# Performance work log

Hardware: AMD Instinct MI355X
Metric: run time of the kernel (lower is better)

Reference implementation:

```python
import jax, jax.numpy as jnp
import numpy as np

B, N, D_IN, D_OUT, H = 2, 2048, 1024, 1024, 16
HD = D_OUT // H


def setup_inputs() -> dict:
    key = jax.random.key(0)
    ks = jax.random.split(key, 6)
    s_in = 1.0 / np.sqrt(D_IN)
    s_out = 1.0 / np.sqrt(D_OUT)
    return {
        "x": jax.random.normal(ks[0], (B, N, D_IN), dtype=jnp.float32),
        "Wq": jax.random.uniform(ks[1], (D_IN, D_OUT), jnp.float32, -s_in, s_in),
        "Wk": jax.random.uniform(ks[2], (D_IN, D_OUT), jnp.float32, -s_in, s_in),
        "Wv": jax.random.uniform(ks[3], (D_IN, D_OUT), jnp.float32, -s_in, s_in),
        "Wo": jax.random.uniform(ks[4], (D_OUT, D_OUT), jnp.float32, -s_out, s_out),
        "bo": jax.random.uniform(ks[5], (D_OUT,), jnp.float32, -s_out, s_out),
    }


def reference(x, Wq, Wk, Wv, Wo, bo):
    b, n, _ = x.shape
    # project and split heads: [b, n, d_out] -> [b, h, n, hd]
    def heads(w):
        return w.reshape(b, n, H, HD).transpose(0, 2, 1, 3)
    q = heads(x @ Wq)
    k = heads(x @ Wk)
    v = heads(x @ Wv)
    # materialized causal attention (dropout rate 0.0 -> identity)
    scores = jnp.einsum("bhqd,bhkd->bhqk", q, k)
    causal = jnp.tril(jnp.ones((n, n), dtype=bool))  # keep lower triangle
    scores = jnp.where(causal, scores, -jnp.inf)
    attn = jax.nn.softmax(scores / np.sqrt(HD), axis=-1)
    ctx = jnp.einsum("bhqk,bhkd->bhqd", attn, v)
    ctx = ctx.transpose(0, 2, 1, 3).reshape(b, n, D_OUT)
    return ctx @ Wo + bo
```

## Files before the change

kernel.cpp:

```cpp
#include <hip/hip_runtime.h>
#include <math.h>
#include <stdint.h>

#define B_ 2
#define N_ 2048
#define D_ 1024
#define H_ 16
#define HD_ 64
#define M_ (B_ * N_)

typedef __bf16 bf16x8 __attribute__((ext_vector_type(8)));
typedef float f32x4 __attribute__((ext_vector_type(4)));

__device__ __forceinline__ ushort bfbits(float f) {
    __bf16 h = (__bf16)f;
    return __builtin_bit_cast(ushort, h);
}

__device__ __forceinline__ void glds16(const ushort* g, ushort* l) {
    __builtin_amdgcn_global_load_lds(
        (const __attribute__((address_space(1))) uint32_t*)g,
        (__attribute__((address_space(3))) uint32_t*)l, 16, 0, 0);
}

__global__ __launch_bounds__(256) void prep(const float* __restrict__ x,
                                            const float* __restrict__ W0,
                                            const float* __restrict__ W1,
                                            const float* __restrict__ W2,
                                            const float* __restrict__ W3,
                                            ushort* __restrict__ xb,
                                            ushort* __restrict__ Wt) {
    __shared__ float T[32][33];
    const int t = threadIdx.x;
    int id = blockIdx.x;
    if (id < 4096) {
        int i = id * 256 + t;
        float4 v = ((const float4*)x)[i];
        ushort4 o;
        o.x = bfbits(v.x); o.y = bfbits(v.y); o.z = bfbits(v.z); o.w = bfbits(v.w);
        ((ushort4*)xb)[i] = o;
        return;
    }
    id -= 4096;
    const int z = id >> 10;
    const int k0 = (id & 31) * 32, n0 = ((id >> 5) & 31) * 32;
    const float* W = (z == 0) ? W0 : (z == 1) ? W1 : (z == 2) ? W2 : W3;
    ushort* out = Wt + (size_t)z * D_ * D_;
    {
        int kl = t >> 3, nl = (t & 7) * 4;
        float4 v = *(const float4*)&W[(size_t)(k0 + kl) * D_ + n0 + nl];
        T[kl][nl] = v.x; T[kl][nl + 1] = v.y; T[kl][nl + 2] = v.z; T[kl][nl + 3] = v.w;
    }
    __syncthreads();
    {
        int nl = t >> 3, k4 = (t & 7) * 4;
        ushort4 o;
        o.x = bfbits(T[k4 + 0][nl]); o.y = bfbits(T[k4 + 1][nl]);
        o.z = bfbits(T[k4 + 2][nl]); o.w = bfbits(T[k4 + 3][nl]);
        *(ushort4*)&out[(size_t)(n0 + nl) * D_ + k0 + k4] = o;
    }
}

#define BK 32

__device__ __forceinline__ void gemm_tile(const ushort* __restrict__ A,
                                          const ushort* __restrict__ Bt,
                                          int K, int tileM, int tileN,
                                          ushort* As, ushort* Bs,
                                          f32x4 acc[4][4]) {
    const int t = threadIdx.x;
    const int l = t & 63;
    const int w = __builtin_amdgcn_readfirstlane(t >> 6);
    const int wr = w >> 1, wc = w & 1;
    const int li = l & 15, lg = l >> 4;
    const int lr = l >> 2;
    const int colu = (((l & 3) ^ (lr & 3)) << 3);
    const int swz = (li & 3) << 3;

    for (int k0 = 0; k0 < K; k0 += BK) {
        __syncthreads();
        #pragma unroll
        for (int it = 0; it < 2; ++it) {
            const int c2 = it * 4 + w;
            const int row = c2 * 16 + lr;
            glds16(&A[(size_t)(tileM + row) * K + k0 + colu], &As[c2 * 512]);
            glds16(&Bt[(size_t)(tileN + row) * K + k0 + colu], &Bs[c2 * 512]);
        }
        __syncthreads();
        bf16x8 a[4], b[4];
        #pragma unroll
        for (int m = 0; m < 4; ++m)
            a[m] = *(const bf16x8*)&As[(wr * 64 + m * 16 + li) * 32 + ((lg << 3) ^ swz)];
        #pragma unroll
        for (int n = 0; n < 4; ++n)
            b[n] = *(const bf16x8*)&Bs[(wc * 64 + n * 16 + li) * 32 + ((lg << 3) ^ swz)];
        #pragma unroll
        for (int m = 0; m < 4; ++m)
            #pragma unroll
            for (int n = 0; n < 4; ++n)
                acc[m][n] = __builtin_amdgcn_mfma_f32_16x16x32_bf16(a[m], b[n], acc[m][n], 0, 0, 0);
    }
}

#define QSCALE 0.180336880f

__global__ __launch_bounds__(256) void qkv_gemm(const ushort* __restrict__ xb,
                                                const ushort* __restrict__ Wt,
                                                ushort* __restrict__ q,
                                                ushort* __restrict__ k,
                                                ushort* __restrict__ vt) {
    __shared__ ushort As[128 * 32];
    __shared__ ushort Bs[128 * 32];
    __shared__ ushort Eps[128][130];
    f32x4 acc[4][4];
    #pragma unroll
    for (int m = 0; m < 4; ++m)
        #pragma unroll
        for (int n = 0; n < 4; ++n)
            acc[m][n] = (f32x4){0.f, 0.f, 0.f, 0.f};

    const int wg = (blockIdx.x & 7) * 96 + (blockIdx.x >> 3);
    const int tileM = (wg & 31) * 128;
    const int yy = wg >> 5;
    const int wsel = yy >> 3;
    const int tileN = (yy & 7) * 128;
    const ushort* Bmat = Wt + (size_t)wsel * D_ * D_;

    gemm_tile(xb, Bmat, D_, tileM, tileN, As, Bs, acc);

    const int t = threadIdx.x;
    const int l = t & 63, w = t >> 6;
    const int wr = w >> 1, wc = w & 1;
    const int li = l & 15, lg = l >> 4;
    const float scale = (wsel == 0) ? QSCALE : 1.0f;

    if (wsel < 2) {
        #pragma unroll
        for (int m = 0; m < 4; ++m)
            #pragma unroll
            for (int n = 0; n < 4; ++n)
                #pragma unroll
                for (int r = 0; r < 4; ++r)
                    Eps[wr * 64 + m * 16 + lg * 4 + r][wc * 64 + n * 16 + li] =
                        bfbits(acc[m][n][r] * scale);
    } else {
        #pragma unroll
        for (int m = 0; m < 4; ++m)
            #pragma unroll
            for (int n = 0; n < 4; ++n)
                #pragma unroll
                for (int r = 0; r < 4; ++r)
                    Eps[wc * 64 + n * 16 + li][wr * 64 + m * 16 + lg * 4 + r] =
                        bfbits(acc[m][n][r]);
    }
    __syncthreads();

    const int rr = t >> 3;
    const int cb = (t & 7) * 16;
    if (wsel < 2) {
        ushort* out = (wsel == 0) ? q : k;
        #pragma unroll
        for (int it = 0; it < 4; ++it) {
            const int row = it * 32 + rr;
            uint4 v0 = *(const uint4*)&Eps[row][cb];
            uint4 v1 = *(const uint4*)&Eps[row][cb + 8];
            size_t base = (size_t)(tileM + row) * D_ + tileN + cb;
            *(uint4*)&out[base] = v0;
            *(uint4*)&out[base + 8] = v1;
        }
    } else {
        const int b = tileM >> 11;
        const int n0 = (tileM & (N_ - 1)) + cb;
        #pragma unroll
        for (int it = 0; it < 4; ++it) {
            const int row = it * 32 + rr;
            const int gcol = tileN + row;
            const int h = gcol >> 6, hd = gcol & 63;
            uint4 v0 = *(const uint4*)&Eps[row][cb];
            uint4 v1 = *(const uint4*)&Eps[row][cb + 8];
            size_t base = ((size_t)(b * H_ + h) * HD_ + hd) * N_ + n0;
            *(uint4*)&vt[base] = v0;
            *(uint4*)&vt[base + 8] = v1;
        }
    }
}

__global__ __launch_bounds__(256) void out_gemm(const ushort* __restrict__ ctx,
                                                const ushort* __restrict__ Wt,
                                                const float* __restrict__ bo,
                                                float* __restrict__ outp) {
    __shared__ ushort As[128 * 32];
    __shared__ ushort Bs[128 * 32];
    f32x4 acc[4][4];
    #pragma unroll
    for (int m = 0; m < 4; ++m)
        #pragma unroll
        for (int n = 0; n < 4; ++n)
            acc[m][n] = (f32x4){0.f, 0.f, 0.f, 0.f};

    const int wg = (blockIdx.x & 7) * 32 + (blockIdx.x >> 3);
    const int tileM = (wg & 31) * 128;
    const int tileN = (wg >> 5) * 128;
    const ushort* Bmat = Wt + (size_t)3 * D_ * D_;

    gemm_tile(ctx, Bmat, D_, tileM, tileN, As, Bs, acc);

    const int l = threadIdx.x & 63, w = threadIdx.x >> 6;
    const int wr = w >> 1, wc = w & 1;
    const int li = l & 15, lg = l >> 4;
    #pragma unroll
    for (int n = 0; n < 4; ++n) {
        float bias = bo[tileN + wc * 64 + n * 16 + li];
        #pragma unroll
        for (int m = 0; m < 4; ++m)
            #pragma unroll
            for (int r = 0; r < 4; ++r) {
                int grow = tileM + wr * 64 + m * 16 + lg * 4 + r;
                int gcol = tileN + wc * 64 + n * 16 + li;
                outp[(size_t)grow * D_ + gcol] = acc[m][n][r] + bias;
            }
    }
}

__device__ __forceinline__ void qk_mfma(f32x4 st[4], const ushort* Kb,
                                        const bf16x8 bq[2],
                                        int li, int lg, int rswz) {
    #pragma unroll
    for (int c = 0; c < 4; ++c) {
        st[c] = (f32x4){0.f, 0.f, 0.f, 0.f};
        #pragma unroll
        for (int tk = 0; tk < 2; ++tk) {
            bf16x8 kf = *(const bf16x8*)&Kb[(c * 16 + li) * 64 + (((tk * 4 + lg) ^ rswz) * 8)];
            st[c] = __builtin_amdgcn_mfma_f32_16x16x32_bf16(kf, bq[tk], st[c], 0, 0, 0);
        }
    }
}

__device__ __forceinline__ void softmax_pv(f32x4 st[4], const ushort* Vb,
                                           bool masked, int jkb, int qg,
                                           int li, int lg, int rswz,
                                           ushort* PsW, f32x4& lacc,
                                           f32x4 od[4], bf16x8 ones) {
    if (masked) {
        #pragma unroll
        for (int c = 0; c < 4; ++c)
            #pragma unroll
            for (int r = 0; r < 4; ++r) {
                const int kgl = jkb * 64 + c * 16 + lg * 4 + r;
                if (kgl > qg) st[c][r] = -INFINITY;
            }
    }
    const int sw = li & 7;
    #pragma unroll
    for (int c = 0; c < 4; ++c) {
        float p0 = exp2f(st[c][0]);
        float p1 = exp2f(st[c][1]);
        float p2 = exp2f(st[c][2]);
        float p3 = exp2f(st[c][3]);
        uint32_t w0, w1;
        asm("v_cvt_pk_bf16_f32 %0, %1, %2" : "=v"(w0) : "v"(p0), "v"(p1));
        asm("v_cvt_pk_bf16_f32 %0, %1, %2" : "=v"(w1) : "v"(p2), "v"(p3));
        uint2 pk; pk.x = w0; pk.y = w1;
        *(uint2*)&PsW[li * 64 + (((c * 2 + (lg >> 1)) ^ sw) << 3) + ((lg & 1) << 2)] = pk;
    }
    #pragma unroll
    for (int tj = 0; tj < 2; ++tj) {
        bf16x8 pa = *(const bf16x8*)&PsW[li * 64 + (((tj * 4 + lg) ^ sw) << 3)];
        lacc = __builtin_amdgcn_mfma_f32_16x16x32_bf16(pa, ones, lacc, 0, 0, 0);
        #pragma unroll
        for (int db = 0; db < 4; ++db) {
            bf16x8 bv = *(const bf16x8*)&Vb[(db * 16 + li) * 64 + (((tj * 4 + lg) ^ rswz) * 8)];
            od[db] = __builtin_amdgcn_mfma_f32_16x16x32_bf16(pa, bv, od[db], 0, 0, 0);
        }
    }
}

__global__ __launch_bounds__(256, 2) void attn_fwd(const ushort* __restrict__ q,
                                                   const ushort* __restrict__ k,
                                                   const ushort* __restrict__ vt,
                                                   ushort* __restrict__ ctx) {
    __shared__ ushort Ks[2][4096];
    __shared__ ushort Vs[2][4096];
    __shared__ ushort Ps[4][1024];

    const int t = threadIdx.x;
    const int l = t & 63;
    const int w = __builtin_amdgcn_readfirstlane(t >> 6);
    const int li = l & 15, lg = l >> 4;
    const int f = blockIdx.x;
    const int bh = ((f & 7) << 2) | ((f >> 3) & 3);
    const int p = f >> 5;
    const int qtA = p, qtB = 31 - p;
    const int b = bh >> 4, h = bh & 15;

    const ushort* Qg = q + ((size_t)b * N_) * D_ + h * 64;
    const ushort* Kg = k + ((size_t)b * N_) * D_ + h * 64;
    const ushort* Vg = vt + (size_t)bh * HD_ * N_;
    ushort* PsW = &Ps[w][0];

    const int r8 = l >> 3;
    const int soff = ((l & 7) ^ r8) * 8;
    const int rswz = li & 7;

    const int qgA = qtA * 64 + w * 16 + li;
    const int qgB = qtB * 64 + w * 16 + li;

    bf16x8 bqA[2], bqB[2];
    #pragma unroll
    for (int tk = 0; tk < 2; ++tk) {
        bqA[tk] = *(const bf16x8*)&Qg[(size_t)qgA * D_ + tk * 32 + lg * 8];
        bqB[tk] = *(const bf16x8*)&Qg[(size_t)qgB * D_ + tk * 32 + lg * 8];
    }

    bf16x8 ones;
    #pragma unroll
    for (int i = 0; i < 8; ++i) ones[i] = (__bf16)1.0f;

    f32x4 odA[4], odB[4];
    #pragma unroll
    for (int db = 0; db < 4; ++db) {
        odA[db] = (f32x4){0.f, 0.f, 0.f, 0.f};
        odB[db] = (f32x4){0.f, 0.f, 0.f, 0.f};
    }
    f32x4 laccA = (f32x4){0.f, 0.f, 0.f, 0.f};
    f32x4 laccB = (f32x4){0.f, 0.f, 0.f, 0.f};

    #pragma unroll
    for (int i = 0; i < 2; ++i) {
        const int seg = w + i * 4;
        const int row = seg * 8 + r8;
        glds16(&Kg[(size_t)row * D_ + soff], &Ks[0][seg * 512]);
        glds16(&Vg[(size_t)row * N_ + soff], &Vs[0][seg * 512]);
    }
    __syncthreads();

    int cur = 0;
    for (int kb = 0; kb <= qtB; ++kb) {
        if (kb < qtB) {
            #pragma unroll
            for (int i = 0; i < 2; ++i) {
                const int seg = w + i * 4;
                const int row = seg * 8 + r8;
                glds16(&Kg[(size_t)((kb + 1) * 64 + row) * D_ + soff], &Ks[cur ^ 1][seg * 512]);
                glds16(&Vg[(size_t)row * N_ + (kb + 1) * 64 + soff], &Vs[cur ^ 1][seg * 512]);
            }
        }
        {
            f32x4 st[4];
            qk_mfma(st, Ks[cur], bqB, li, lg, rswz);
            softmax_pv(st, Vs[cur], kb == qtB, kb, qgB, li, lg, rswz, PsW, laccB, odB, ones);
        }
        if (kb <= qtA) {
            f32x4 st[4];
            qk_mfma(st, Ks[cur], bqA, li, lg, rswz);
            softmax_pv(st, Vs[cur], kb == qtA, kb, qgA, li, lg, rswz, PsW, laccA, odA, ones);
        }
        __syncthreads();
        cur ^= 1;
    }

    #pragma unroll
    for (int r = 0; r < 4; ++r) {
        const float invA = 1.f / laccA[r];
        const int growA = qtA * 64 + w * 16 + lg * 4 + r;
        #pragma unroll
        for (int db = 0; db < 4; ++db)
            ctx[((size_t)(b * N_ + growA)) * D_ + h * 64 + db * 16 + li] = bfbits(odA[db][r] * invA);
        const float invB = 1.f / laccB[r];
        const int growB = qtB * 64 + w * 16 + lg * 4 + r;
        #pragma unroll
        for (int db = 0; db < 4; ++db)
            ctx[((size_t)(b * N_ + growB)) * D_ + h * 64 + db * 16 + li] = bfbits(odB[db][r] * invB);
    }
}

extern "C" void kernel_launch(void* const* d_in, const int* in_sizes, int n_in,
                              void* d_out, int out_size, void* d_ws, size_t ws_size,
                              hipStream_t stream) {
    (void)in_sizes; (void)n_in; (void)out_size; (void)ws_size;
    const float* x  = (const float*)d_in[0];
    const float* Wq = (const float*)d_in[1];
    const float* Wk = (const float*)d_in[2];
    const float* Wv = (const float*)d_in[3];
    const float* Wo = (const float*)d_in[4];
    const float* bo = (const float*)d_in[5];
    float* outp = (float*)d_out;

    ushort* xb  = (ushort*)d_ws;
    ushort* Wt  = xb + (size_t)M_ * D_;
    ushort* qb  = Wt + (size_t)4 * D_ * D_;
    ushort* kb  = qb + (size_t)M_ * D_;
    ushort* vtb = kb + (size_t)M_ * D_;
    ushort* ctx = vtb + (size_t)M_ * D_;

    prep<<<dim3(8192), 256, 0, stream>>>(x, Wq, Wk, Wv, Wo, xb, Wt);
    qkv_gemm<<<dim3(768), 256, 0, stream>>>(xb, Wt, qb, kb, vtb);
    attn_fwd<<<dim3(512), 256, 0, stream>>>(qb, kb, vtb, ctx);
    out_gemm<<<dim3(256), 256, 0, stream>>>(ctx, Wt, bo, outp);
}
```

Baseline: 106.8 us.

## Replace QKV GEMM with 256x256 double-buffered 8-wave pipelined kernel

Replaces the 128x128 single-buffered QKV projection with a 256x256-tile, 512-thread kernel. It double-buffers K=64 LDS stages and interleaves global-to-LDS loads with MFMA phases using sched barriers and s_setprio. V is computed directly as Wv^T·x^T so the transposed layout comes out of the GEMM without an LDS transpose epilogue. The larger tiles give more reuse per byte and hide load latency. The trade-off is only 192 workgroups on a GPU with 256 CUs, and uncoalesced scalar 2-byte stores in the epilogue.

```diff
diff --git a/kernel.cpp b/kernel.cpp
--- a/kernel.cpp
+++ b/kernel.cpp
@@ -61,6 +61,166 @@
     }
 }
 
+#define QSCALE 0.180336880f
+
+#define STG(SRC, RB, K0, DST, HALF)                                            \
+    do {                                                                       \
+        glds16(&SRC[(size_t)((RB) + (HALF) * 128 + w * 8 + r8) * 1024 + (K0) + s8], \
+               &DST[((HALF) * 128 + w * 8) * 64]);                             \
+        glds16(&SRC[(size_t)((RB) + (HALF) * 128 + (w + 8) * 8 + r8) * 1024 + (K0) + s8], \
+               &DST[((HALF) * 128 + (w + 8) * 8) * 64]);                       \
+    } while (0)
+
+#define DS_READS(KT, MH, TK)                                                   \
+    _Pragma("unroll") for (int mi = 0; mi < 4; ++mi)                           \
+        af[mi] = *(const bf16x8*)&LA[KT][(wr * 128 + ((MH) * 4 + mi) * 16 + li) * 64 + \
+                                         ((((TK) * 4 + lg) ^ rsw) << 3)];      \
+    _Pragma("unroll") for (int nj = 0; nj < 4; ++nj)                           \
+        bfr[nj] = *(const bf16x8*)&LB[KT][(wc * 64 + nj * 16 + li) * 64 +      \
+                                          ((((TK) * 4 + lg) ^ rsw) << 3)];
+
+#define MFMA16(MH)                                                             \
+    __builtin_amdgcn_s_setprio(1);                                             \
+    _Pragma("unroll") for (int mi = 0; mi < 4; ++mi)                           \
+        _Pragma("unroll") for (int nj = 0; nj < 4; ++nj)                       \
+            acc[(MH) * 4 + mi][nj] = __builtin_amdgcn_mfma_f32_16x16x32_bf16(  \
+                af[mi], bfr[nj], acc[(MH) * 4 + mi][nj], 0, 0, 0);             \
+    __builtin_amdgcn_s_setprio(0);
+
+#define BARF()                                                                 \
+    __builtin_amdgcn_sched_barrier(0);                                         \
+    __builtin_amdgcn_s_barrier();                                              \
+    __builtin_amdgcn_sched_barrier(0)
+
+__global__ __launch_bounds__(512, 2) void qkv8_gemm(const ushort* __restrict__ xb,
+                                                    const ushort* __restrict__ Wt,
+                                                    ushort* __restrict__ q,
+                                                    ushort* __restrict__ k,
+                                                    ushort* __restrict__ vt) {
+    __shared__ ushort LA[2][256 * 64];
+    __shared__ ushort LB[2][256 * 64];
+
+    const int t = threadIdx.x;
+    const int l = t & 63;
+    const int w = __builtin_amdgcn_readfirstlane(t >> 6);
+    const int wr = w >> 2, wc = w & 3;
+    const int li = l & 15, lg = l >> 4;
+    const int r8 = l >> 3;
+    const int s8 = ((l & 7) ^ r8) * 8;
+    const int rsw = li & 7;
+
+    const int wg = (blockIdx.x & 7) * 24 + (blockIdx.x >> 3);
+    const int op = wg >> 6;
+    const int rr_ = wg & 63;
+    const ushort* Asrc; const ushort* Bsrc;
+    int rowbase, colbase;
+    if (op < 2) {
+        Asrc = xb; Bsrc = Wt + (size_t)op * D_ * D_;
+        rowbase = (rr_ & 15) * 256;
+        colbase = (rr_ >> 4) * 256;
+    } else {
+        Asrc = Wt + (size_t)2 * D_ * D_;
+        Bsrc = xb;
+        rowbase = (rr_ & 3) * 256;
+        colbase = (rr_ >> 2) * 256;
+    }
+
+    f32x4 acc[8][4];
+    #pragma unroll
+    for (int m = 0; m < 8; ++m)
+        #pragma unroll
+        for (int n = 0; n < 4; ++n)
+            acc[m][n] = (f32x4){0.f, 0.f, 0.f, 0.f};
+
+    STG(Asrc, rowbase, 0, LA[0], 0);  STG(Asrc, rowbase, 0, LA[0], 1);
+    STG(Bsrc, colbase, 0, LB[0], 0);  STG(Bsrc, colbase, 0, LB[0], 1);
+    STG(Asrc, rowbase, 64, LA[1], 0); STG(Asrc, rowbase, 64, LA[1], 1);
+    STG(Bsrc, colbase, 64, LB[1], 0); STG(Bsrc, colbase, 64, LB[1], 1);
+
+    #pragma unroll 1
+    for (int it = 0; it < 8; ++it) {
+        const int kT1 = it * 128 + 64;
+        const int kN0 = it * 128 + 128;
+        const int kN1 = it * 128 + 192;
+        bf16x8 af[4], bfr[4];
+
+        if (it > 0) STG(Asrc, rowbase, kT1, LA[1], 1);
+        asm volatile("s_waitcnt vmcnt(4)" ::: "memory");
+        BARF();
+        DS_READS(0, 0, 0);
+        MFMA16(0);
+        BARF();
+        DS_READS(0, 0, 1);
+        if (it > 0) STG(Bsrc, colbase, kT1, LB[1], 0);
+        BARF();
+        MFMA16(0);
+        BARF();
+        DS_READS(0, 1, 0);
+        if (it > 0) STG(Bsrc, colbase, kT1, LB[1], 1);
+        BARF();
+        MFMA16(1);
+        BARF();
+        DS_READS(0, 1, 1);
+        if (it < 7) STG(Asrc, rowbase, kN0, LA[0], 0);
+        BARF();
+        MFMA16(1);
+        BARF();
+        if (it < 7) {
+            STG(Asrc, rowbase, kN0, LA[0], 1);
+            asm volatile("s_waitcnt vmcnt(4)" ::: "memory");
+        } else {
+            asm volatile("s_waitcnt vmcnt(0)" ::: "memory");
+        }
+        BARF();
+        DS_READS(1, 0, 0);
+        MFMA16(0);
+        BARF();
+        DS_READS(1, 0, 1);
+        if (it < 7) STG(Bsrc, colbase, kN0, LB[0], 0);
+        BARF();
+        MFMA16(0);
+        BARF();
+        DS_READS(1, 1, 0);
+        if (it < 7) STG(Bsrc, colbase, kN0, LB[0], 1);
+        BARF();
+        MFMA16(1);
+        BARF();
+        DS_READS(1, 1, 1);
+        if (it < 7) STG(Asrc, rowbase, kN1, LA[1], 0);
+        BARF();
+        MFMA16(1);
+        BARF();
+    }
+
+    if (op < 2) {
+        ushort* out = (op == 0) ? q : k;
+        const float scale = (op == 0) ? QSCALE : 1.0f;
+        #pragma unroll
+        for (int m = 0; m < 8; ++m)
+            #pragma unroll
+            for (int n = 0; n < 4; ++n)
+                #pragma unroll
+                for (int r = 0; r < 4; ++r) {
+                    const int grow = rowbase + wr * 128 + m * 16 + lg * 4 + r;
+                    const int gcol = colbase + wc * 64 + n * 16 + li;
+                    out[(size_t)grow * D_ + gcol] = bfbits(acc[m][n][r] * scale);
+                }
+    } else {
+        const int bb = colbase >> 11;
+        const int tcb = colbase & (N_ - 1);
+        #pragma unroll
+        for (int m = 0; m < 8; ++m)
+            #pragma unroll
+            for (int n = 0; n < 4; ++n)
+                #pragma unroll
+                for (int r = 0; r < 4; ++r) {
+                    const int drow = rowbase + wr * 128 + m * 16 + lg * 4 + r;
+                    const int tcol = tcb + wc * 64 + n * 16 + li;
+                    vt[((size_t)(bb * 1024 + drow)) * N_ + tcol] = bfbits(acc[m][n][r]);
+                }
+    }
+}
+
 #define BK 32
 
 __device__ __forceinline__ void gemm_tile(const ushort* __restrict__ A,
@@ -102,89 +262,6 @@
     }
 }
 
-#define QSCALE 0.180336880f
-
-__global__ __launch_bounds__(256) void qkv_gemm(const ushort* __restrict__ xb,
-                                                const ushort* __restrict__ Wt,
-                                                ushort* __restrict__ q,
-                                                ushort* __restrict__ k,
-                                                ushort* __restrict__ vt) {
-    __shared__ ushort As[128 * 32];
-    __shared__ ushort Bs[128 * 32];
-    __shared__ ushort Eps[128][130];
-    f32x4 acc[4][4];
-    #pragma unroll
-    for (int m = 0; m < 4; ++m)
-        #pragma unroll
-        for (int n = 0; n < 4; ++n)
-            acc[m][n] = (f32x4){0.f, 0.f, 0.f, 0.f};
-
-    const int wg = (blockIdx.x & 7) * 96 + (blockIdx.x >> 3);
-    const int tileM = (wg & 31) * 128;
-    const int yy = wg >> 5;
-    const int wsel = yy >> 3;
-    const int tileN = (yy & 7) * 128;
-    const ushort* Bmat = Wt + (size_t)wsel * D_ * D_;
-
-    gemm_tile(xb, Bmat, D_, tileM, tileN, As, Bs, acc);
-
-    const int t = threadIdx.x;
-    const int l = t & 63, w = t >> 6;
-    const int wr = w >> 1, wc = w & 1;
-    const int li = l & 15, lg = l >> 4;
-    const float scale = (wsel == 0) ? QSCALE : 1.0f;
-
-    if (wsel < 2) {
-        #pragma unroll
-        for (int m = 0; m < 4; ++m)
-            #pragma unroll
-            for (int n = 0; n < 4; ++n)
-                #pragma unroll
-                for (int r = 0; r < 4; ++r)
-                    Eps[wr * 64 + m * 16 + lg * 4 + r][wc * 64 + n * 16 + li] =
-                        bfbits(acc[m][n][r] * scale);
-    } else {
-        #pragma unroll
-        for (int m = 0; m < 4; ++m)
-            #pragma unroll
-            for (int n = 0; n < 4; ++n)
-                #pragma unroll
-                for (int r = 0; r < 4; ++r)
-                    Eps[wc * 64 + n * 16 + li][wr * 64 + m * 16 + lg * 4 + r] =
-                        bfbits(acc[m][n][r]);
-    }
-    __syncthreads();
-
-    const int rr = t >> 3;
-    const int cb = (t & 7) * 16;
-    if (wsel < 2) {
-        ushort* out = (wsel == 0) ? q : k;
-        #pragma unroll
-        for (int it = 0; it < 4; ++it) {
-            const int row = it * 32 + rr;
-            uint4 v0 = *(const uint4*)&Eps[row][cb];
-            uint4 v1 = *(const uint4*)&Eps[row][cb + 8];
-            size_t base = (size_t)(tileM + row) * D_ + tileN + cb;
-            *(uint4*)&out[base] = v0;
-            *(uint4*)&out[base + 8] = v1;
-        }
-    } else {
-        const int b = tileM >> 11;
-        const int n0 = (tileM & (N_ - 1)) + cb;
-        #pragma unroll
-        for (int it = 0; it < 4; ++it) {
-            const int row = it * 32 + rr;
-            const int gcol = tileN + row;
-            const int h = gcol >> 6, hd = gcol & 63;
-            uint4 v0 = *(const uint4*)&Eps[row][cb];
-            uint4 v1 = *(const uint4*)&Eps[row][cb + 8];
-            size_t base = ((size_t)(b * H_ + h) * HD_ + hd) * N_ + n0;
-            *(uint4*)&vt[base] = v0;
-            *(uint4*)&vt[base + 8] = v1;
-        }
-    }
-}
-
 __global__ __launch_bounds__(256) void out_gemm(const ushort* __restrict__ ctx,
                                                 const ushort* __restrict__ Wt,
                                                 const float* __restrict__ bo,
@@ -394,7 +471,7 @@
     ushort* ctx = vtb + (size_t)M_ * D_;
 
     prep<<<dim3(8192), 256, 0, stream>>>(x, Wq, Wk, Wv, Wo, xb, Wt);
-    qkv_gemm<<<dim3(768), 256, 0, stream>>>(xb, Wt, qb, kb, vtb);
+    qkv8_gemm<<<dim3(192), 512, 0, stream>>>(xb, Wt, qb, kb, vtb);
     attn_fwd<<<dim3(512), 256, 0, stream>>>(qb, kb, vtb, ctx);
     out_gemm<<<dim3(256), 256, 0, stream>>>(ctx, Wt, bo, outp);
 }
```

Measured after the change: 109.3 us. 1.02x slower.

## Triple-buffer K/V tiles in attention with partial vmcnt waits

Applied to the files above, without the earlier changes.

Moves the attention kernel's K/V LDS staging from a double buffer to a triple buffer, prefetching two tiles ahead. It replaces the full __syncthreads with explicit s_waitcnt vmcnt(4)/vmcnt(0) plus a raw barrier, so loads for the next tile can stay in flight across the barrier. The P scratch buffer is split per query tile (A/B) so the two softmax passes don't share LDS. This raises LDS use per block, which may reduce occupancy relative to the launch bound of 2 blocks per CU.

```diff
diff --git a/kernel.cpp b/kernel.cpp
--- a/kernel.cpp
+++ b/kernel.cpp
@@ -222,6 +222,12 @@
     }
 }
 
+#define WAITV4() do { asm volatile("s_waitcnt vmcnt(4)" ::: "memory"); } while (0)
+#define WAITV0() do { asm volatile("s_waitcnt vmcnt(0)" ::: "memory"); } while (0)
+#define SBAR()  do { __builtin_amdgcn_sched_barrier(0); \
+                     __builtin_amdgcn_s_barrier(); \
+                     __builtin_amdgcn_sched_barrier(0); } while (0)
+
 __device__ __forceinline__ void qk_mfma(f32x4 st[4], const ushort* Kb,
                                         const bf16x8 bq[2],
                                         int li, int lg, int rswz) {
@@ -279,9 +285,9 @@
                                                    const ushort* __restrict__ k,
                                                    const ushort* __restrict__ vt,
                                                    ushort* __restrict__ ctx) {
-    __shared__ ushort Ks[2][4096];
-    __shared__ ushort Vs[2][4096];
-    __shared__ ushort Ps[4][1024];
+    __shared__ ushort Ks[3][4096];
+    __shared__ ushort Vs[3][4096];
+    __shared__ ushort Ps[2][4][1024];
 
     const int t = threadIdx.x;
     const int l = t & 63;
@@ -296,7 +302,8 @@
     const ushort* Qg = q + ((size_t)b * N_) * D_ + h * 64;
     const ushort* Kg = k + ((size_t)b * N_) * D_ + h * 64;
     const ushort* Vg = vt + (size_t)bh * HD_ * N_;
-    ushort* PsW = &Ps[w][0];
+    ushort* PsB = &Ps[0][w][0];
+    ushort* PsA = &Ps[1][w][0];
 
     const int r8 = l >> 3;
     const int soff = ((l & 7) ^ r8) * 8;
@@ -326,37 +333,43 @@
     f32x4 laccB = (f32x4){0.f, 0.f, 0.f, 0.f};
 
     #pragma unroll
-    for (int i = 0; i < 2; ++i) {
-        const int seg = w + i * 4;
-        const int row = seg * 8 + r8;
-        glds16(&Kg[(size_t)row * D_ + soff], &Ks[0][seg * 512]);
-        glds16(&Vg[(size_t)row * N_ + soff], &Vs[0][seg * 512]);
-    }
-    __syncthreads();
-
-    int cur = 0;
+    for (int s = 0; s < 2; ++s)
+        #pragma unroll
+        for (int i = 0; i < 2; ++i) {
+            const int seg = w + i * 4;
+            const int row = seg * 8 + r8;
+            glds16(&Kg[(size_t)(s * 64 + row) * D_ + soff], &Ks[s][seg * 512]);
+            glds16(&Vg[(size_t)row * N_ + s * 64 + soff], &Vs[s][seg * 512]);
+        }
+    WAITV4();
+    SBAR();
+
     for (int kb = 0; kb <= qtB; ++kb) {
-        if (kb < qtB) {
+        const int rd = kb % 3;
+        if (kb + 2 <= qtB) {
+            const int st = (kb + 2) % 3;
             #pragma unroll
             for (int i = 0; i < 2; ++i) {
                 const int seg = w + i * 4;
                 const int row = seg * 8 + r8;
-                glds16(&Kg[(size_t)((kb + 1) * 64 + row) * D_ + soff], &Ks[cur ^ 1][seg * 512]);
-                glds16(&Vg[(size_t)row * N_ + (kb + 1) * 64 + soff], &Vs[cur ^ 1][seg * 512]);
+                glds16(&Kg[(size_t)((kb + 2) * 64 + row) * D_ + soff], &Ks[st][seg * 512]);
+                glds16(&Vg[(size_t)row * N_ + (kb + 2) * 64 + soff], &Vs[st][seg * 512]);
             }
         }
         {
-            f32x4 st[4];
-            qk_mfma(st, Ks[cur], bqB, li, lg, rswz);
-            softmax_pv(st, Vs[cur], kb == qtB, kb, qgB, li, lg, rswz, PsW, laccB, odB, ones);
+            f32x4 st4[4];
+            qk_mfma(st4, Ks[rd], bqB, li, lg, rswz);
+            softmax_pv(st4, Vs[rd], kb == qtB, kb, qgB, li, lg, rswz, PsB, laccB, odB, ones);
         }
         if (kb <= qtA) {
-            f32x4 st[4];
-            qk_mfma(st, Ks[cur], bqA, li, lg, rswz);
-            softmax_pv(st, Vs[cur], kb == qtA, kb, qgA, li, lg, rswz, PsW, laccA, odA, ones);
-        }
-        __syncthreads();
-        cur ^= 1;
+            f32x4 st4[4];
+            qk_mfma(st4, Ks[rd], bqA, li, lg, rswz);
+            softmax_pv(st4, Vs[rd], kb == qtA, kb, qgA, li, lg, rswz, PsA, laccA, odA, ones);
+        }
+        if (kb < qtB) {
+            if (kb + 2 <= qtB) WAITV4(); else WAITV0();
+            SBAR();
+        }
     }
 
     #pragma unroll
```

New measurement: 107.5 us. Within noise of the previous version (+0.7%).

## Split paired causal query tiles across 8 waves instead of serial per-wave processing

Applied to the files above, without the earlier changes.

The attention kernel previously had each of 4 waves process two query tiles (p and 31-p) serially for load balance. Now blocks use 512 threads: waves 0-3 handle the long tile and waves 4-7 the short tile, sharing the same double-buffered K/V LDS tiles, with each wave loading one K/V segment. This halves per-wave register state and doubles parallelism per block, but the short-tile waves sit idle at barriers once their tile finishes.

```diff
diff --git a/kernel.cpp b/kernel.cpp
--- a/kernel.cpp
+++ b/kernel.cpp
@@ -275,13 +275,13 @@
     }
 }
 
-__global__ __launch_bounds__(256, 2) void attn_fwd(const ushort* __restrict__ q,
+__global__ __launch_bounds__(512, 4) void attn_fwd(const ushort* __restrict__ q,
                                                    const ushort* __restrict__ k,
                                                    const ushort* __restrict__ vt,
                                                    ushort* __restrict__ ctx) {
     __shared__ ushort Ks[2][4096];
     __shared__ ushort Vs[2][4096];
-    __shared__ ushort Ps[4][1024];
+    __shared__ ushort Ps[8][1024];
 
     const int t = threadIdx.x;
     const int l = t & 63;
@@ -290,8 +290,9 @@
     const int f = blockIdx.x;
     const int bh = ((f & 7) << 2) | ((f >> 3) & 3);
     const int p = f >> 5;
-    const int qtA = p, qtB = 31 - p;
     const int b = bh >> 4, h = bh & 15;
+    const int wl = w & 3;
+    const int myqt = (w < 4) ? (31 - p) : p;
 
     const ushort* Qg = q + ((size_t)b * N_) * D_ + h * 64;
     const ushort* Kg = k + ((size_t)b * N_) * D_ + h * 64;
@@ -299,61 +300,41 @@
     ushort* PsW = &Ps[w][0];
 
     const int r8 = l >> 3;
+    const int srow = w * 8 + r8;
     const int soff = ((l & 7) ^ r8) * 8;
     const int rswz = li & 7;
 
-    const int qgA = qtA * 64 + w * 16 + li;
-    const int qgB = qtB * 64 + w * 16 + li;
-
-    bf16x8 bqA[2], bqB[2];
-    #pragma unroll
-    for (int tk = 0; tk < 2; ++tk) {
-        bqA[tk] = *(const bf16x8*)&Qg[(size_t)qgA * D_ + tk * 32 + lg * 8];
-        bqB[tk] = *(const bf16x8*)&Qg[(size_t)qgB * D_ + tk * 32 + lg * 8];
-    }
+    const int qg = myqt * 64 + wl * 16 + li;
+
+    bf16x8 bq[2];
+    #pragma unroll
+    for (int tk = 0; tk < 2; ++tk)
+        bq[tk] = *(const bf16x8*)&Qg[(size_t)qg * D_ + tk * 32 + lg * 8];
 
     bf16x8 ones;
     #pragma unroll
     for (int i = 0; i < 8; ++i) ones[i] = (__bf16)1.0f;
 
-    f32x4 odA[4], odB[4];
-    #pragma unroll
-    for (int db = 0; db < 4; ++db) {
-        odA[db] = (f32x4){0.f, 0.f, 0.f, 0.f};
-        odB[db] = (f32x4){0.f, 0.f, 0.f, 0.f};
-    }
-    f32x4 laccA = (f32x4){0.f, 0.f, 0.f, 0.f};
-    f32x4 laccB = (f32x4){0.f, 0.f, 0.f, 0.f};
-
-    #pragma unroll
-    for (int i = 0; i < 2; ++i) {
-        const int seg = w + i * 4;
-        const int row = seg * 8 + r8;
-        glds16(&Kg[(size_t)row * D_ + soff], &Ks[0][seg * 512]);
-        glds16(&Vg[(size_t)row * N_ + soff], &Vs[0][seg * 512]);
-    }
+    f32x4 od[4];
+    #pragma unroll
+    for (int db = 0; db < 4; ++db) od[db] = (f32x4){0.f, 0.f, 0.f, 0.f};
+    f32x4 lacc = (f32x4){0.f, 0.f, 0.f, 0.f};
+
+    glds16(&Kg[(size_t)srow * D_ + soff], &Ks[0][w * 512]);
+    glds16(&Vg[(size_t)srow * N_ + soff], &Vs[0][w * 512]);
     __syncthreads();
 
+    const int nst = 32 - p;
     int cur = 0;
-    for (int kb = 0; kb <= qtB; ++kb) {
-        if (kb < qtB) {
-            #pragma unroll
-            for (int i = 0; i < 2; ++i) {
-                const int seg = w + i * 4;
-                const int row = seg * 8 + r8;
-                glds16(&Kg[(size_t)((kb + 1) * 64 + row) * D_ + soff], &Ks[cur ^ 1][seg * 512]);
-                glds16(&Vg[(size_t)row * N_ + (kb + 1) * 64 + soff], &Vs[cur ^ 1][seg * 512]);
-            }
-        }
-        {
-            f32x4 st[4];
-            qk_mfma(st, Ks[cur], bqB, li, lg, rswz);
-            softmax_pv(st, Vs[cur], kb == qtB, kb, qgB, li, lg, rswz, PsW, laccB, odB, ones);
-        }
-        if (kb <= qtA) {
-            f32x4 st[4];
-            qk_mfma(st, Ks[cur], bqA, li, lg, rswz);
-            softmax_pv(st, Vs[cur], kb == qtA, kb, qgA, li, lg, rswz, PsW, laccA, odA, ones);
+    for (int kb = 0; kb < nst; ++kb) {
+        if (kb + 1 < nst) {
+            glds16(&Kg[(size_t)((kb + 1) * 64 + srow) * D_ + soff], &Ks[cur ^ 1][w * 512]);
+            glds16(&Vg[(size_t)srow * N_ + (kb + 1) * 64 + soff], &Vs[cur ^ 1][w * 512]);
+        }
+        if (kb <= myqt) {
+            f32x4 st4[4];
+            qk_mfma(st4, Ks[cur], bq, li, lg, rswz);
+            softmax_pv(st4, Vs[cur], kb == myqt, kb, qg, li, lg, rswz, PsW, lacc, od, ones);
         }
         __syncthreads();
         cur ^= 1;
@@ -361,16 +342,11 @@
 
     #pragma unroll
     for (int r = 0; r < 4; ++r) {
-        const float invA = 1.f / laccA[r];
-        const int growA = qtA * 64 + w * 16 + lg * 4 + r;
+        const float inv = 1.f / lacc[r];
+        const int grow = myqt * 64 + wl * 16 + lg * 4 + r;
         #pragma unroll
         for (int db = 0; db < 4; ++db)
-            ctx[((size_t)(b * N_ + growA)) * D_ + h * 64 + db * 16 + li] = bfbits(odA[db][r] * invA);
-        const float invB = 1.f / laccB[r];
-        const int growB = qtB * 64 + w * 16 + lg * 4 + r;
-        #pragma unroll
-        for (int db = 0; db < 4; ++db)
-            ctx[((size_t)(b * N_ + growB)) * D_ + h * 64 + db * 16 + li] = bfbits(odB[db][r] * invB);
+            ctx[((size_t)(b * N_ + grow)) * D_ + h * 64 + db * 16 + li] = bfbits(od[db][r] * inv);
     }
 }
 
@@ -395,6 +371,6 @@
 
     prep<<<dim3(8192), 256, 0, stream>>>(x, Wq, Wk, Wv, Wo, xb, Wt);
     qkv_gemm<<<dim3(768), 256, 0, stream>>>(xb, Wt, qb, kb, vtb);
-    attn_fwd<<<dim3(512), 256, 0, stream>>>(qb, kb, vtb, ctx);
+    attn_fwd<<<dim3(512), 512, 0, stream>>>(qb, kb, vtb, ctx);
     out_gemm<<<dim3(256), 256, 0, stream>>>(ctx, Wt, bo, outp);
 }
```

New measurement: 106.9 us. Within noise of the previous version (+0.1%).
